# Kernel optimization log

Measured on AMD Instinct MI355X. Metric: run time of the kernel, lower is better.

The kernel has to match this reference:

```python
import jax, jax.numpy as jnp
import numpy as np

EPS = 1e-5
N_NODES = 100000

def _glorot(key, shape):
    lim = float(np.sqrt(6.0 / (shape[0] + shape[1])))
    return jax.random.uniform(key, shape, jnp.float32, -lim, lim)

def setup_inputs() -> dict:
    key = jax.random.key(0)
    ks = jax.random.split(key, 16)
    x = jax.random.normal(ks[0], (N_NODES, 64), jnp.float32)
    edge_index = jax.random.randint(ks[1], (2, 1600000), 0, N_NODES, jnp.int64)
    chans = [64, 128, 128, 1]
    inp = {"x": x, "edge_index": edge_index}
    for i in range(3):
        ci, co = chans[i], chans[i + 1]
        inp[f"Wl{i}"] = _glorot(ks[2 + 3 * i], (ci, co))
        inp[f"bl{i}"] = jnp.zeros((co,), jnp.float32)
        inp[f"Wr{i}"] = _glorot(ks[3 + 3 * i], (ci, co))
    inp["g0"] = jnp.ones((128,), jnp.float32); inp["be0"] = jnp.zeros((128,), jnp.float32)
    inp["g1"] = jnp.ones((128,), jnp.float32); inp["be1"] = jnp.zeros((128,), jnp.float32)
    inp["wF"] = _glorot(ks[11], (1, 1))
    inp["bF"] = jnp.zeros((1,), jnp.float32)
    return inp

def _sage_conv(x, src, dst, Wl, bl, Wr):
    # mean aggregation over incoming edges (PyG SAGEConv default)
    msg = x[src]                                                   # [E, Cin]
    agg = jax.ops.segment_sum(msg, dst, num_segments=N_NODES)      # [N, Cin]
    cnt = jax.ops.segment_sum(jnp.ones((src.shape[0], 1), x.dtype), dst, num_segments=N_NODES)
    agg = agg / jnp.maximum(cnt, 1.0)
    return agg @ Wl + bl + x @ Wr

def _batchnorm(x, g, b):
    mu = jnp.mean(x, axis=0)
    var = jnp.mean(jnp.square(x - mu), axis=0)  # biased, training-mode BN
    return (x - mu) * jax.lax.rsqrt(var + EPS) * g + b

def reference(x, edge_index, Wl0, bl0, Wr0, Wl1, bl1, Wr1, Wl2, bl2, Wr2, g0, be0, g1, be1, wF, bF):
    src, dst = edge_index[0], edge_index[1]
    h = _sage_conv(x, src, dst, Wl0, bl0, Wr0)
    h = jax.nn.relu(_batchnorm(h, g0, be0))
    h = _sage_conv(h, src, dst, Wl1, bl1, Wr1)
    h = jax.nn.relu(_batchnorm(h, g1, be1))
    h = _sage_conv(h, src, dst, Wl2, bl2, Wr2)        # activation 'None', no BN
    h = h @ wF + bF                                    # final Linear(1,1)
    return jax.nn.sigmoid(h)
```

## Files before the change

kernel.cpp:

```cpp
#include <hip/hip_runtime.h>
#include <math.h>

#define BN_EPS 1e-5f
#define SCAN_CHUNK 4096

typedef __attribute__((ext_vector_type(8))) short bf16x8;
typedef __attribute__((ext_vector_type(4))) float f32x4;

__device__ __forceinline__ unsigned short f2bf(float f) {
    unsigned int u = __float_as_uint(f);
    u = (u + 0x7fffu + ((u >> 16) & 1u)) >> 16;
    return (unsigned short)u;
}
__device__ __forceinline__ float bflo(unsigned int u) { return __uint_as_float(u << 16); }
__device__ __forceinline__ float bfhi(unsigned int u) { return __uint_as_float(u & 0xffff0000u); }

__global__ void to_bf16_k(const float* __restrict__ in, unsigned short* __restrict__ out, int n4) {
    int i = blockIdx.x * blockDim.x + threadIdx.x;
    if (i >= n4) return;
    float4 v = ((const float4*)in)[i];
    ((ushort4*)out)[i] = make_ushort4(f2bf(v.x), f2bf(v.y), f2bf(v.z), f2bf(v.w));
}

__global__ void count_edges_sliced_k(const int* __restrict__ dst, int E,
                                     int* __restrict__ cnt, int nper) {
    const int slice = blockIdx.x & 7;
    const int lo = slice * nper;
    const int hi = lo + nper;
    int i = (blockIdx.x >> 3) * blockDim.x + threadIdx.x;
    int stride = (gridDim.x >> 3) * blockDim.x;
    for (int e = i; e < E; e += stride) {
        int d = dst[e];
        if (d >= lo && d < hi) atomicAdd(&cnt[d], 1);
    }
}

__device__ __forceinline__ int wave_incl_scan(int v, int lane) {
#pragma unroll
    for (int d = 1; d < 64; d <<= 1) {
        int u = __shfl_up(v, d);
        if (lane >= d) v += u;
    }
    return v;
}

__global__ void block_sum_k(const int* __restrict__ cnt, int N, int* __restrict__ bsum) {
    const int t = threadIdx.x;
    const int base = blockIdx.x * SCAN_CHUNK;
    int s = 0;
    for (int i = t; i < SCAN_CHUNK; i += 256) {
        int idx = base + i;
        if (idx < N) s += cnt[idx];
    }
    const int lane = t & 63, wid = t >> 6;
#pragma unroll
    for (int d = 32; d; d >>= 1) s += __shfl_down(s, d);
    __shared__ int ws[4];
    if (lane == 0) ws[wid] = s;
    __syncthreads();
    if (t == 0) bsum[blockIdx.x] = ws[0] + ws[1] + ws[2] + ws[3];
}

__global__ void scan_bsums_k(int* __restrict__ bsum, int nb) {
    int lane = threadIdx.x;
    int v = (lane < nb) ? bsum[lane] : 0;
    int incl = wave_incl_scan(v, lane);
    if (lane < nb) bsum[lane] = incl - v;
}

__global__ void scan_write_k(const int* __restrict__ cnt, const int* __restrict__ bsum, int N,
                             int* __restrict__ off, int* __restrict__ cursor,
                             float* __restrict__ inv) {
    const int t = threadIdx.x;
    const int base = blockIdx.x * SCAN_CHUNK;
    const int idx0 = base + t * 16;
    int pre[16];
    int s = 0;
#pragma unroll
    for (int j = 0; j < 16; ++j) {
        int i = idx0 + j;
        int c = (i < N) ? cnt[i] : 0;
        pre[j] = s;
        s += c;
    }
    const int lane = t & 63, wid = t >> 6;
    int incl = wave_incl_scan(s, lane);
    __shared__ int ws[4];
    if (lane == 63) ws[wid] = incl;
    __syncthreads();
    if (t == 0) {
        int a = 0;
#pragma unroll
        for (int w = 0; w < 4; ++w) { int tmp = ws[w]; ws[w] = a; a += tmp; }
    }
    __syncthreads();
    const int tbase = bsum[blockIdx.x] + (incl - s) + ws[wid];
#pragma unroll
    for (int j = 0; j < 16; ++j) {
        int i = idx0 + j;
        if (i < N) {
            int c = cnt[i];
            int o = tbase + pre[j];
            off[i] = o;
            cursor[i] = o;
            inv[i] = 1.0f / fmaxf((float)c, 1.0f);
        }
    }
}

__global__ void csr_fill_sliced_k(const int* __restrict__ src, const int* __restrict__ dst,
                                  const int* __restrict__ off, int E,
                                  int* __restrict__ cursor, int* __restrict__ csr,
                                  float slice_scale) {
    const int slice = blockIdx.x & 7;
    const int g = blockIdx.x >> 3;
    const int ng = gridDim.x >> 3;
    int i = g * blockDim.x + threadIdx.x;
    int stride = ng * blockDim.x;
    for (int e = i; e < E; e += stride) {
        int d = dst[e];
        int o = off[d];
        int s = (int)((float)o * slice_scale);
        s = s > 7 ? 7 : s;
        if (s == slice) {
            int pos = atomicAdd(&cursor[d], 1);
            csr[pos] = src[e];
        }
    }
}

__global__ void wfrag_build_k(const float* __restrict__ Wl, const float* __restrict__ Wr,
                              int CIN, int KIT, unsigned short* __restrict__ wf) {
    int t = blockIdx.x * blockDim.x + threadIdx.x;
    int lane = t & 63;
    int q = t >> 6;
    if (q >= 8 * KIT) return;
    int kit = q % KIT;
    int ct = q / KIT;
    int col = ct * 16 + (lane & 15);
    bf16x8 v;
#pragma unroll
    for (int j = 0; j < 8; ++j) {
        int kg = kit * 32 + ((lane >> 4) << 3) + j;
        float f = (kg < CIN) ? Wl[(size_t)kg * 128 + col] : Wr[(size_t)(kg - CIN) * 128 + col];
        v[j] = (short)f2bf(f);
    }
    ((bf16x8*)wf)[q * 64 + lane] = v;
}

template<int CIN>
__launch_bounds__(256)
__global__ void fused_sage_k(const unsigned short* __restrict__ feat,
                             const unsigned short* __restrict__ xin,
                             const int* __restrict__ csr, const int* __restrict__ off,
                             const int* __restrict__ endp, const float* __restrict__ inv,
                             const unsigned short* __restrict__ wfrag,
                             const float* __restrict__ bl,
                             unsigned short* __restrict__ outb,
                             float* __restrict__ stats8, int N) {
    constexpr int KT = 2 * CIN;
    constexpr int KIT = KT / 32;
    __shared__ unsigned short sA[32 * KT];

    const int t = threadIdx.x;
    const int lane = t & 63, wave = t >> 6;
    const int rowbase = blockIdx.x * 32;
    const unsigned int* f32p = (const unsigned int*)feat;

    constexpr int CH8 = CIN / 8;
    for (int i = t; i < 32 * CH8; i += 256) {
        int r = i / CH8, q = i % CH8;
        if (rowbase + r < N) {
            uint4 v = ((const uint4*)(xin + (size_t)(rowbase + r) * CIN))[q];
            int byte = ((r * KT + CIN + q * 8) * 2) ^ ((r & 7) << 4);
            *(uint4*)((char*)sA + byte) = v;
        }
    }

#pragma unroll
    for (int rr = 0; rr < 8; ++rr) {
        int r = wave * 8 + rr;
        int n = rowbase + r;
        if (n < N) {
            const int o = off[n], eend = endp[n];
            float a0 = 0.f, a1 = 0.f;
            if constexpr (CIN == 128) {
                int e = o;
                for (; e + 3 < eend; e += 4) {
                    unsigned int u0 = f32p[(size_t)csr[e]     * 64 + lane];
                    unsigned int u1 = f32p[(size_t)csr[e + 1] * 64 + lane];
                    unsigned int u2 = f32p[(size_t)csr[e + 2] * 64 + lane];
                    unsigned int u3 = f32p[(size_t)csr[e + 3] * 64 + lane];
                    a0 += (bflo(u0) + bflo(u1)) + (bflo(u2) + bflo(u3));
                    a1 += (bfhi(u0) + bfhi(u1)) + (bfhi(u2) + bfhi(u3));
                }
                for (; e < eend; ++e) {
                    unsigned int u = f32p[(size_t)csr[e] * 64 + lane];
                    a0 += bflo(u); a1 += bfhi(u);
                }
                float iv = inv[n];
                unsigned int pk = (unsigned int)f2bf(a0 * iv) | ((unsigned int)f2bf(a1 * iv) << 16);
                int byte = ((r * KT + 2 * lane) * 2) ^ ((r & 7) << 4);
                *(unsigned int*)((char*)sA + byte) = pk;
            } else {
                const int c = lane & 31, g = lane >> 5;
                int e = o + g;
                for (; e + 7 < eend; e += 8) {
                    unsigned int u0 = f32p[(size_t)csr[e]     * 32 + c];
                    unsigned int u1 = f32p[(size_t)csr[e + 2] * 32 + c];
                    unsigned int u2 = f32p[(size_t)csr[e + 4] * 32 + c];
                    unsigned int u3 = f32p[(size_t)csr[e + 6] * 32 + c];
                    a0 += (bflo(u0) + bflo(u1)) + (bflo(u2) + bflo(u3));
                    a1 += (bfhi(u0) + bfhi(u1)) + (bfhi(u2) + bfhi(u3));
                }
                for (; e < eend; e += 2) {
                    unsigned int u = f32p[(size_t)csr[e] * 32 + c];
                    a0 += bflo(u); a1 += bfhi(u);
                }
                a0 += __shfl_xor(a0, 32);
                a1 += __shfl_xor(a1, 32);
                if (g == 0) {
                    float iv = inv[n];
                    unsigned int pk = (unsigned int)f2bf(a0 * iv) | ((unsigned int)f2bf(a1 * iv) << 16);
                    int byte = ((r * KT + 2 * c) * 2) ^ ((r & 7) << 4);
                    *(unsigned int*)((char*)sA + byte) = pk;
                }
            }
        }
    }
    __syncthreads();

    f32x4 acc00 = {0.f,0.f,0.f,0.f}, acc01 = acc00, acc10 = acc00, acc11 = acc00;
    const int koff = (lane >> 4) << 4;
    const int swz = (lane & 7) << 4;
    const int base0 = (lane & 15) * KT * 2 + koff;
    const int base1 = (16 + (lane & 15)) * KT * 2 + koff;
    const bf16x8* wf8 = (const bf16x8*)wfrag;
    const int bq0 = (wave * 2 + 0) * KIT;
    const int bq1 = (wave * 2 + 1) * KIT;

#pragma unroll
    for (int kit = 0; kit < KIT; ++kit) {
        bf16x8 fa0 = *(const bf16x8*)((const char*)sA + ((base0 + kit * 64) ^ swz));
        bf16x8 fa1 = *(const bf16x8*)((const char*)sA + ((base1 + kit * 64) ^ swz));
        bf16x8 fb0 = wf8[(bq0 + kit) * 64 + lane];
        bf16x8 fb1 = wf8[(bq1 + kit) * 64 + lane];
        acc00 = __builtin_amdgcn_mfma_f32_16x16x32_bf16(fa0, fb0, acc00, 0, 0, 0);
        acc01 = __builtin_amdgcn_mfma_f32_16x16x32_bf16(fa0, fb1, acc01, 0, 0, 0);
        acc10 = __builtin_amdgcn_mfma_f32_16x16x32_bf16(fa1, fb0, acc10, 0, 0, 0);
        acc11 = __builtin_amdgcn_mfma_f32_16x16x32_bf16(fa1, fb1, acc11, 0, 0, 0);
    }

    const int c0 = wave * 32 + (lane & 15);
    const int c1 = c0 + 16;
    const float b0 = bl[c0], b1 = bl[c1];
    float sum0 = 0.f, sq0 = 0.f, sum1 = 0.f, sq1 = 0.f;
    const int row0base = rowbase + ((lane >> 4) << 2);
#pragma unroll
    for (int r = 0; r < 4; ++r) {
        int row0 = row0base + r, row1 = row0 + 16;
        float v00 = acc00[r] + b0, v01 = acc01[r] + b1;
        float v10 = acc10[r] + b0, v11 = acc11[r] + b1;
        if (row0 < N) {
            outb[(size_t)row0 * 128 + c0] = f2bf(v00);
            outb[(size_t)row0 * 128 + c1] = f2bf(v01);
            sum0 += v00; sq0 += v00 * v00; sum1 += v01; sq1 += v01 * v01;
        }
        if (row1 < N) {
            outb[(size_t)row1 * 128 + c0] = f2bf(v10);
            outb[(size_t)row1 * 128 + c1] = f2bf(v11);
            sum0 += v10; sq0 += v10 * v10; sum1 += v11; sq1 += v11 * v11;
        }
    }
#pragma unroll
    for (int m = 16; m < 64; m <<= 1) {
        sum0 += __shfl_xor(sum0, m); sq0 += __shfl_xor(sq0, m);
        sum1 += __shfl_xor(sum1, m); sq1 += __shfl_xor(sq1, m);
    }
    if (lane < 16) {
        float* st = stats8 + (blockIdx.x & 7) * 256;
        atomicAdd(&st[c0], sum0);
        atomicAdd(&st[128 + c0], sq0);
        atomicAdd(&st[c1], sum1);
        atomicAdd(&st[128 + c1], sq1);
    }
}

__global__ void bn_finalize8_k(const float* __restrict__ g, const float* __restrict__ be,
                               const float* __restrict__ stats8, float* __restrict__ sfin, int N) {
    int c = threadIdx.x;
    if (c < 128) {
        float s = 0.f, s2 = 0.f;
#pragma unroll
        for (int k = 0; k < 8; ++k) { s += stats8[k * 256 + c]; s2 += stats8[k * 256 + 128 + c]; }
        float mu = s / (float)N;
        float var = s2 / (float)N - mu * mu;
        float sc = g[c] * rsqrtf(var + BN_EPS);
        sfin[c] = sc;
        sfin[128 + c] = be[c] - mu * sc;
    }
}

__global__ void bn_apply_inplace_k(unsigned short* __restrict__ hb, const float* __restrict__ sfin,
                                   int total_u4) {
    int i = blockIdx.x * blockDim.x + threadIdx.x;
    int stride = gridDim.x * blockDim.x;
    for (; i < total_u4; i += stride) {
        uint4 v = ((uint4*)hb)[i];
        int c0 = (i & 15) * 8;
        unsigned int w[4] = {v.x, v.y, v.z, v.w};
#pragma unroll
        for (int j = 0; j < 4; ++j) {
            float lo = fmaxf(bflo(w[j]) * sfin[c0 + 2*j]     + sfin[128 + c0 + 2*j],     0.f);
            float hi = fmaxf(bfhi(w[j]) * sfin[c0 + 2*j + 1] + sfin[128 + c0 + 2*j + 1], 0.f);
            w[j] = (unsigned int)f2bf(lo) | ((unsigned int)f2bf(hi) << 16);
        }
        ((uint4*)hb)[i] = make_uint4(w[0], w[1], w[2], w[3]);
    }
}

__global__ void bn_apply_p_k(unsigned short* __restrict__ hb, const float* __restrict__ sfin,
                             const float* __restrict__ Wl2, float* __restrict__ p, int N) {
    const int lane = threadIdx.x & 63;
    const int n = (int)((blockIdx.x * (long long)blockDim.x + threadIdx.x) >> 6);
    if (n >= N) return;
    const float2 sc = ((const float2*)sfin)[lane];
    const float2 sh = ((const float2*)(sfin + 128))[lane];
    const float2 w  = ((const float2*)Wl2)[lane];
    unsigned int u = ((unsigned int*)(hb + (size_t)n * 128))[lane];
    float vx = fmaxf(bflo(u) * sc.x + sh.x, 0.f);
    float vy = fmaxf(bfhi(u) * sc.y + sh.y, 0.f);
    ((unsigned int*)(hb + (size_t)n * 128))[lane] = (unsigned int)f2bf(vx) | ((unsigned int)f2bf(vy) << 16);
    float s = vx * w.x + vy * w.y;
#pragma unroll
    for (int o = 32; o; o >>= 1) s += __shfl_down(s, o);
    if (lane == 0) p[n] = s;
}

__global__ void layer2_final_k(const unsigned short* __restrict__ hb, const float* __restrict__ p,
                               const int* __restrict__ csr, const int* __restrict__ off,
                               const int* __restrict__ endp, const float* __restrict__ inv,
                               const float* __restrict__ Wr2, const float* __restrict__ bl2,
                               const float* __restrict__ wF, const float* __restrict__ bF,
                               float* __restrict__ out, int N) {
    const int lane = threadIdx.x & 63;
    const int n = (int)((blockIdx.x * (long long)blockDim.x + threadIdx.x) >> 6);
    if (n >= N) return;
    float2 w = ((const float2*)Wr2)[lane];
    unsigned int u = ((const unsigned int*)(hb + (size_t)n * 128))[lane];
    float dotp = bflo(u) * w.x + bfhi(u) * w.y;
    float ps = 0.f;
    const int o = off[n], e_end = endp[n];
    for (int e = o + lane; e < e_end; e += 64) ps += p[csr[e]];
    float s = dotp + ps * inv[n];
#pragma unroll
    for (int ow = 32; ow; ow >>= 1) s += __shfl_down(s, ow);
    if (lane == 0) {
        float z = (s + bl2[0]) * wF[0] + bF[0];
        out[n] = 1.f / (1.f + expf(-z));
    }
}

extern "C" void kernel_launch(void* const* d_in, const int* in_sizes, int n_in,
                              void* d_out, int out_size, void* d_ws, size_t ws_size,
                              hipStream_t stream) {
    const float* x   = (const float*)d_in[0];
    const int*   ei  = (const int*)d_in[1];
    const int E = in_sizes[1] / 2;
    const int N = in_sizes[0] / 64;
    const int* src = ei;
    const int* dst = ei + E;
    const float* Wl0 = (const float*)d_in[2];
    const float* bl0 = (const float*)d_in[3];
    const float* Wr0 = (const float*)d_in[4];
    const float* Wl1 = (const float*)d_in[5];
    const float* bl1 = (const float*)d_in[6];
    const float* Wr1 = (const float*)d_in[7];
    const float* Wl2 = (const float*)d_in[8];
    const float* bl2 = (const float*)d_in[9];
    const float* Wr2 = (const float*)d_in[10];
    const float* g0  = (const float*)d_in[11];
    const float* be0 = (const float*)d_in[12];
    const float* g1  = (const float*)d_in[13];
    const float* be1 = (const float*)d_in[14];
    const float* wF  = (const float*)d_in[15];
    const float* bF  = (const float*)d_in[16];

    char* wp = (char*)d_ws;
    unsigned short* h0   = (unsigned short*)wp;  wp += (size_t)N * 128 * 2;
    unsigned short* h1   = (unsigned short*)wp;  wp += (size_t)N * 128 * 2;
    unsigned short* xb   = (unsigned short*)wp;  wp += (size_t)N * 64 * 2;
    int*   cnt    = (int*)wp;    wp += (size_t)N * 4;
    int*   off    = (int*)wp;    wp += (size_t)N * 4;
    int*   cursor = (int*)wp;    wp += (size_t)N * 4;
    float* inv    = (float*)wp;  wp += (size_t)N * 4;
    int*   csr    = (int*)wp;    wp += (size_t)E * 4;
    float* stats8a = (float*)wp; wp += 2048 * 4;
    float* stats8b = (float*)wp; wp += 2048 * 4;
    float* sfin0   = (float*)wp; wp += 256 * 4;
    float* sfin1   = (float*)wp; wp += 256 * 4;
    int*   bsum    = (int*)wp;   wp += 64 * 4;
    unsigned short* wf0 = (unsigned short*)wp; wp += 8 * 4 * 64 * 8 * 2;
    unsigned short* wf1 = (unsigned short*)wp; wp += 8 * 8 * 64 * 8 * 2;
    float* p = (float*)cnt;
    float* out = (float*)d_out;

    const int gemm_grid = (N + 31) / 32;
    const int wave_grid = (N + 3) / 4;
    const int nb = (N + SCAN_CHUNK - 1) / SCAN_CHUNK;

    wfrag_build_k<<<(8 * 4 * 64 + 255) / 256, 256, 0, stream>>>(Wl0, Wr0, 64, 4, wf0);
    wfrag_build_k<<<(8 * 8 * 64 + 255) / 256, 256, 0, stream>>>(Wl1, Wr1, 128, 8, wf1);
    to_bf16_k<<<(N * 16 + 255) / 256, 256, 0, stream>>>(x, xb, N * 16);
    hipMemsetAsync(stats8a, 0, (2048 + 2048 + 256 + 256) * sizeof(float), stream);

    hipMemsetAsync(cnt, 0, (size_t)N * sizeof(int), stream);
    count_edges_sliced_k<<<2048, 256, 0, stream>>>(dst, E, cnt, (N + 7) / 8);
    block_sum_k<<<nb, 256, 0, stream>>>(cnt, N, bsum);
    scan_bsums_k<<<1, 64, 0, stream>>>(bsum, nb);
    scan_write_k<<<nb, 256, 0, stream>>>(cnt, bsum, N, off, cursor, inv);
    csr_fill_sliced_k<<<2048, 256, 0, stream>>>(src, dst, off, E, cursor, csr, 8.0f / (float)E);

    fused_sage_k<64><<<gemm_grid, 256, 0, stream>>>(xb, xb, csr, off, cursor, inv,
                                                    wf0, bl0, h0, stats8a, N);
    bn_finalize8_k<<<1, 128, 0, stream>>>(g0, be0, stats8a, sfin0, N);
    bn_apply_inplace_k<<<2048, 256, 0, stream>>>(h0, sfin0, N * 16);

    fused_sage_k<128><<<gemm_grid, 256, 0, stream>>>(h0, h0, csr, off, cursor, inv,
                                                     wf1, bl1, h1, stats8b, N);
    bn_finalize8_k<<<1, 128, 0, stream>>>(g1, be1, stats8b, sfin1, N);
    bn_apply_p_k<<<wave_grid, 256, 0, stream>>>(h1, sfin1, Wl2, p, N);

    layer2_final_k<<<wave_grid, 256, 0, stream>>>(h1, p, csr, off, cursor, inv,
                                                  Wr2, bl2, wF, bF, out, N);
}
```

Measured before the change: 433.8 us.

## Fuse BN0 finalize and apply into layer-1 gather, merge scan kernels

Folds the first BatchNorm finalize and ReLU into the layer-1 fused SAGE kernel, so normalization is applied on the fly to gathered neighbor features and self features. This removes the separate finalize and in-place apply passes over h0. The separate block-sum scan kernel is also merged into scan_write_k, and the gather loops are unrolled to 8 loads with two accumulator pairs. The cost is extra FMA and max work per gathered element (16 edges per node), since BN is now recomputed per edge instead of once per node, plus a redundant stats reduction in every block.

```diff
diff --git a/kernel.cpp b/kernel.cpp
--- a/kernel.cpp
+++ b/kernel.cpp
@@ -14,6 +14,18 @@
 }
 __device__ __forceinline__ float bflo(unsigned int u) { return __uint_as_float(u << 16); }
 __device__ __forceinline__ float bfhi(unsigned int u) { return __uint_as_float(u & 0xffff0000u); }
+
+template<bool BNIN>
+__device__ __forceinline__ void acc2(unsigned int u, float sc0, float sh0, float sc1, float sh1,
+                                     float& a0, float& a1) {
+    if constexpr (BNIN) {
+        a0 += fmaxf(bflo(u) * sc0 + sh0, 0.f);
+        a1 += fmaxf(bfhi(u) * sc1 + sh1, 0.f);
+    } else {
+        a0 += bflo(u);
+        a1 += bfhi(u);
+    }
+}
 
 __global__ void to_bf16_k(const float* __restrict__ in, unsigned short* __restrict__ out, int n4) {
     int i = blockIdx.x * blockDim.x + threadIdx.x;
@@ -61,17 +73,17 @@
     if (t == 0) bsum[blockIdx.x] = ws[0] + ws[1] + ws[2] + ws[3];
 }
 
-__global__ void scan_bsums_k(int* __restrict__ bsum, int nb) {
-    int lane = threadIdx.x;
-    int v = (lane < nb) ? bsum[lane] : 0;
-    int incl = wave_incl_scan(v, lane);
-    if (lane < nb) bsum[lane] = incl - v;
-}
-
-__global__ void scan_write_k(const int* __restrict__ cnt, const int* __restrict__ bsum, int N,
-                             int* __restrict__ off, int* __restrict__ cursor,
+__global__ void scan_write_k(const int* __restrict__ cnt, const int* __restrict__ bsum, int nb,
+                             int N, int* __restrict__ off, int* __restrict__ cursor,
                              float* __restrict__ inv) {
     const int t = threadIdx.x;
+    __shared__ int ws[4];
+    __shared__ int base_s;
+    if (t < 64) {
+        int v = (t < nb) ? bsum[t] : 0;
+        int incl = wave_incl_scan(v, t);
+        if (t == blockIdx.x) base_s = incl - v;
+    }
     const int base = blockIdx.x * SCAN_CHUNK;
     const int idx0 = base + t * 16;
     int pre[16];
@@ -85,7 +97,6 @@
     }
     const int lane = t & 63, wid = t >> 6;
     int incl = wave_incl_scan(s, lane);
-    __shared__ int ws[4];
     if (lane == 63) ws[wid] = incl;
     __syncthreads();
     if (t == 0) {
@@ -94,7 +105,7 @@
         for (int w = 0; w < 4; ++w) { int tmp = ws[w]; ws[w] = a; a += tmp; }
     }
     __syncthreads();
-    const int tbase = bsum[blockIdx.x] + (incl - s) + ws[wid];
+    const int tbase = base_s + (incl - s) + ws[wid];
 #pragma unroll
     for (int j = 0; j < 16; ++j) {
         int i = idx0 + j;
@@ -148,7 +159,7 @@
     ((bf16x8*)wf)[q * 64 + lane] = v;
 }
 
-template<int CIN>
+template<int CIN, bool BNIN>
 __launch_bounds__(256)
 __global__ void fused_sage_k(const unsigned short* __restrict__ feat,
                              const unsigned short* __restrict__ xin,
@@ -156,25 +167,60 @@
                              const int* __restrict__ endp, const float* __restrict__ inv,
                              const unsigned short* __restrict__ wfrag,
                              const float* __restrict__ bl,
+                             const float* __restrict__ g, const float* __restrict__ be,
+                             const float* __restrict__ stats8in,
                              unsigned short* __restrict__ outb,
-                             float* __restrict__ stats8, int N) {
+                             float* __restrict__ stats8out, int N) {
     constexpr int KT = 2 * CIN;
     constexpr int KIT = KT / 32;
     __shared__ unsigned short sA[32 * KT];
+    __shared__ float sfinS[256];
 
     const int t = threadIdx.x;
     const int lane = t & 63, wave = t >> 6;
     const int rowbase = blockIdx.x * 32;
     const unsigned int* f32p = (const unsigned int*)feat;
+
+    if constexpr (BNIN) {
+        if (t < 128) {
+            float s = 0.f, s2 = 0.f;
+#pragma unroll
+            for (int k = 0; k < 8; ++k) { s += stats8in[k * 256 + t]; s2 += stats8in[k * 256 + 128 + t]; }
+            float mu = s / (float)N;
+            float var = s2 / (float)N - mu * mu;
+            float sc = g[t] * rsqrtf(var + BN_EPS);
+            sfinS[t] = sc;
+            sfinS[128 + t] = be[t] - mu * sc;
+        }
+        __syncthreads();
+    }
 
     constexpr int CH8 = CIN / 8;
     for (int i = t; i < 32 * CH8; i += 256) {
         int r = i / CH8, q = i % CH8;
         if (rowbase + r < N) {
             uint4 v = ((const uint4*)(xin + (size_t)(rowbase + r) * CIN))[q];
+            if constexpr (BNIN) {
+                unsigned int w[4] = {v.x, v.y, v.z, v.w};
+#pragma unroll
+                for (int j = 0; j < 4; ++j) {
+                    int c = q * 8 + 2 * j;
+                    float lo = fmaxf(bflo(w[j]) * sfinS[c]     + sfinS[128 + c],     0.f);
+                    float hi = fmaxf(bfhi(w[j]) * sfinS[c + 1] + sfinS[128 + c + 1], 0.f);
+                    w[j] = (unsigned int)f2bf(lo) | ((unsigned int)f2bf(hi) << 16);
+                }
+                v = make_uint4(w[0], w[1], w[2], w[3]);
+            }
             int byte = ((r * KT + CIN + q * 8) * 2) ^ ((r & 7) << 4);
             *(uint4*)((char*)sA + byte) = v;
         }
+    }
+
+    float sc0 = 1.f, sh0 = 0.f, sc1 = 1.f, sh1 = 0.f;
+    if constexpr (BNIN) {
+        int cc = (CIN == 128) ? (2 * lane) : (2 * (lane & 31));
+        sc0 = sfinS[cc];     sh0 = sfinS[128 + cc];
+        sc1 = sfinS[cc + 1]; sh1 = sfinS[128 + cc + 1];
     }
 
 #pragma unroll
@@ -183,43 +229,85 @@
         int n = rowbase + r;
         if (n < N) {
             const int o = off[n], eend = endp[n];
-            float a0 = 0.f, a1 = 0.f;
+            float a0 = 0.f, a1 = 0.f, b0f = 0.f, b1f = 0.f;
             if constexpr (CIN == 128) {
                 int e = o;
+                for (; e + 7 < eend; e += 8) {
+                    unsigned int u0 = f32p[(size_t)csr[e]     * 64 + lane];
+                    unsigned int u1 = f32p[(size_t)csr[e + 1] * 64 + lane];
+                    unsigned int u2 = f32p[(size_t)csr[e + 2] * 64 + lane];
+                    unsigned int u3 = f32p[(size_t)csr[e + 3] * 64 + lane];
+                    unsigned int u4 = f32p[(size_t)csr[e + 4] * 64 + lane];
+                    unsigned int u5 = f32p[(size_t)csr[e + 5] * 64 + lane];
+                    unsigned int u6 = f32p[(size_t)csr[e + 6] * 64 + lane];
+                    unsigned int u7 = f32p[(size_t)csr[e + 7] * 64 + lane];
+                    acc2<BNIN>(u0, sc0, sh0, sc1, sh1, a0, a1);
+                    acc2<BNIN>(u1, sc0, sh0, sc1, sh1, b0f, b1f);
+                    acc2<BNIN>(u2, sc0, sh0, sc1, sh1, a0, a1);
+                    acc2<BNIN>(u3, sc0, sh0, sc1, sh1, b0f, b1f);
+                    acc2<BNIN>(u4, sc0, sh0, sc1, sh1, a0, a1);
+                    acc2<BNIN>(u5, sc0, sh0, sc1, sh1, b0f, b1f);
+                    acc2<BNIN>(u6, sc0, sh0, sc1, sh1, a0, a1);
+                    acc2<BNIN>(u7, sc0, sh0, sc1, sh1, b0f, b1f);
+                }
                 for (; e + 3 < eend; e += 4) {
                     unsigned int u0 = f32p[(size_t)csr[e]     * 64 + lane];
                     unsigned int u1 = f32p[(size_t)csr[e + 1] * 64 + lane];
                     unsigned int u2 = f32p[(size_t)csr[e + 2] * 64 + lane];
                     unsigned int u3 = f32p[(size_t)csr[e + 3] * 64 + lane];
-                    a0 += (bflo(u0) + bflo(u1)) + (bflo(u2) + bflo(u3));
-                    a1 += (bfhi(u0) + bfhi(u1)) + (bfhi(u2) + bfhi(u3));
+                    acc2<BNIN>(u0, sc0, sh0, sc1, sh1, a0, a1);
+                    acc2<BNIN>(u1, sc0, sh0, sc1, sh1, b0f, b1f);
+                    acc2<BNIN>(u2, sc0, sh0, sc1, sh1, a0, a1);
+                    acc2<BNIN>(u3, sc0, sh0, sc1, sh1, b0f, b1f);
                 }
                 for (; e < eend; ++e) {
                     unsigned int u = f32p[(size_t)csr[e] * 64 + lane];
-                    a0 += bflo(u); a1 += bfhi(u);
-                }
+                    acc2<BNIN>(u, sc0, sh0, sc1, sh1, a0, a1);
+                }
+                a0 += b0f; a1 += b1f;
                 float iv = inv[n];
                 unsigned int pk = (unsigned int)f2bf(a0 * iv) | ((unsigned int)f2bf(a1 * iv) << 16);
                 int byte = ((r * KT + 2 * lane) * 2) ^ ((r & 7) << 4);
                 *(unsigned int*)((char*)sA + byte) = pk;
             } else {
-                const int c = lane & 31, g = lane >> 5;
-                int e = o + g;
-                for (; e + 7 < eend; e += 8) {
+                const int c = lane & 31, g2 = lane >> 5;
+                int e = o + g2;
+                for (; e + 14 < eend; e += 16) {
+                    unsigned int u0 = f32p[(size_t)csr[e]      * 32 + c];
+                    unsigned int u1 = f32p[(size_t)csr[e + 2]  * 32 + c];
+                    unsigned int u2 = f32p[(size_t)csr[e + 4]  * 32 + c];
+                    unsigned int u3 = f32p[(size_t)csr[e + 6]  * 32 + c];
+                    unsigned int u4 = f32p[(size_t)csr[e + 8]  * 32 + c];
+                    unsigned int u5 = f32p[(size_t)csr[e + 10] * 32 + c];
+                    unsigned int u6 = f32p[(size_t)csr[e + 12] * 32 + c];
+                    unsigned int u7 = f32p[(size_t)csr[e + 14] * 32 + c];
+                    acc2<false>(u0, 0, 0, 0, 0, a0, a1);
+                    acc2<false>(u1, 0, 0, 0, 0, b0f, b1f);
+                    acc2<false>(u2, 0, 0, 0, 0, a0, a1);
+                    acc2<false>(u3, 0, 0, 0, 0, b0f, b1f);
+                    acc2<false>(u4, 0, 0, 0, 0, a0, a1);
+                    acc2<false>(u5, 0, 0, 0, 0, b0f, b1f);
+                    acc2<false>(u6, 0, 0, 0, 0, a0, a1);
+                    acc2<false>(u7, 0, 0, 0, 0, b0f, b1f);
+                }
+                for (; e + 6 < eend; e += 8) {
                     unsigned int u0 = f32p[(size_t)csr[e]     * 32 + c];
                     unsigned int u1 = f32p[(size_t)csr[e + 2] * 32 + c];
                     unsigned int u2 = f32p[(size_t)csr[e + 4] * 32 + c];
                     unsigned int u3 = f32p[(size_t)csr[e + 6] * 32 + c];
-                    a0 += (bflo(u0) + bflo(u1)) + (bflo(u2) + bflo(u3));
-                    a1 += (bfhi(u0) + bfhi(u1)) + (bfhi(u2) + bfhi(u3));
+                    acc2<false>(u0, 0, 0, 0, 0, a0, a1);
+                    acc2<false>(u1, 0, 0, 0, 0, b0f, b1f);
+                    acc2<false>(u2, 0, 0, 0, 0, a0, a1);
+                    acc2<false>(u3, 0, 0, 0, 0, b0f, b1f);
                 }
                 for (; e < eend; e += 2) {
                     unsigned int u = f32p[(size_t)csr[e] * 32 + c];
-                    a0 += bflo(u); a1 += bfhi(u);
-                }
+                    acc2<false>(u, 0, 0, 0, 0, a0, a1);
+                }
+                a0 += b0f; a1 += b1f;
                 a0 += __shfl_xor(a0, 32);
                 a1 += __shfl_xor(a1, 32);
-                if (g == 0) {
+                if (g2 == 0) {
                     float iv = inv[n];
                     unsigned int pk = (unsigned int)f2bf(a0 * iv) | ((unsigned int)f2bf(a1 * iv) << 16);
                     int byte = ((r * KT + 2 * c) * 2) ^ ((r & 7) << 4);
@@ -278,7 +366,7 @@
         sum1 += __shfl_xor(sum1, m); sq1 += __shfl_xor(sq1, m);
     }
     if (lane < 16) {
-        float* st = stats8 + (blockIdx.x & 7) * 256;
+        float* st = stats8out + (blockIdx.x & 7) * 256;
         atomicAdd(&st[c0], sum0);
         atomicAdd(&st[128 + c0], sq0);
         atomicAdd(&st[c1], sum1);
@@ -298,24 +386,6 @@
         float sc = g[c] * rsqrtf(var + BN_EPS);
         sfin[c] = sc;
         sfin[128 + c] = be[c] - mu * sc;
-    }
-}
-
-__global__ void bn_apply_inplace_k(unsigned short* __restrict__ hb, const float* __restrict__ sfin,
-                                   int total_u4) {
-    int i = blockIdx.x * blockDim.x + threadIdx.x;
-    int stride = gridDim.x * blockDim.x;
-    for (; i < total_u4; i += stride) {
-        uint4 v = ((uint4*)hb)[i];
-        int c0 = (i & 15) * 8;
-        unsigned int w[4] = {v.x, v.y, v.z, v.w};
-#pragma unroll
-        for (int j = 0; j < 4; ++j) {
-            float lo = fmaxf(bflo(w[j]) * sfin[c0 + 2*j]     + sfin[128 + c0 + 2*j],     0.f);
-            float hi = fmaxf(bfhi(w[j]) * sfin[c0 + 2*j + 1] + sfin[128 + c0 + 2*j + 1], 0.f);
-            w[j] = (unsigned int)f2bf(lo) | ((unsigned int)f2bf(hi) << 16);
-        }
-        ((uint4*)hb)[i] = make_uint4(w[0], w[1], w[2], w[3]);
     }
 }
 
@@ -397,7 +467,6 @@
     int*   csr    = (int*)wp;    wp += (size_t)E * 4;
     float* stats8a = (float*)wp; wp += 2048 * 4;
     float* stats8b = (float*)wp; wp += 2048 * 4;
-    float* sfin0   = (float*)wp; wp += 256 * 4;
     float* sfin1   = (float*)wp; wp += 256 * 4;
     int*   bsum    = (int*)wp;   wp += 64 * 4;
     unsigned short* wf0 = (unsigned short*)wp; wp += 8 * 4 * 64 * 8 * 2;
@@ -412,22 +481,20 @@
     wfrag_build_k<<<(8 * 4 * 64 + 255) / 256, 256, 0, stream>>>(Wl0, Wr0, 64, 4, wf0);
     wfrag_build_k<<<(8 * 8 * 64 + 255) / 256, 256, 0, stream>>>(Wl1, Wr1, 128, 8, wf1);
     to_bf16_k<<<(N * 16 + 255) / 256, 256, 0, stream>>>(x, xb, N * 16);
-    hipMemsetAsync(stats8a, 0, (2048 + 2048 + 256 + 256) * sizeof(float), stream);
+    hipMemsetAsync(stats8a, 0, (2048 + 2048) * sizeof(float), stream);
 
     hipMemsetAsync(cnt, 0, (size_t)N * sizeof(int), stream);
     count_edges_sliced_k<<<2048, 256, 0, stream>>>(dst, E, cnt, (N + 7) / 8);
     block_sum_k<<<nb, 256, 0, stream>>>(cnt, N, bsum);
-    scan_bsums_k<<<1, 64, 0, stream>>>(bsum, nb);
-    scan_write_k<<<nb, 256, 0, stream>>>(cnt, bsum, N, off, cursor, inv);
+    scan_write_k<<<nb, 256, 0, stream>>>(cnt, bsum, nb, N, off, cursor, inv);
     csr_fill_sliced_k<<<2048, 256, 0, stream>>>(src, dst, off, E, cursor, csr, 8.0f / (float)E);
 
-    fused_sage_k<64><<<gemm_grid, 256, 0, stream>>>(xb, xb, csr, off, cursor, inv,
-                                                    wf0, bl0, h0, stats8a, N);
-    bn_finalize8_k<<<1, 128, 0, stream>>>(g0, be0, stats8a, sfin0, N);
-    bn_apply_inplace_k<<<2048, 256, 0, stream>>>(h0, sfin0, N * 16);
-
-    fused_sage_k<128><<<gemm_grid, 256, 0, stream>>>(h0, h0, csr, off, cursor, inv,
-                                                     wf1, bl1, h1, stats8b, N);
+    fused_sage_k<64, false><<<gemm_grid, 256, 0, stream>>>(
+        xb, xb, csr, off, cursor, inv, wf0, bl0, nullptr, nullptr, nullptr, h0, stats8a, N);
+
+    fused_sage_k<128, true><<<gemm_grid, 256, 0, stream>>>(
+        h0, h0, csr, off, cursor, inv, wf1, bl1, g0, be0, stats8a, h1, stats8b, N);
+
     bn_finalize8_k<<<1, 128, 0, stream>>>(g1, be1, stats8b, sfin1, N);
     bn_apply_p_k<<<wave_grid, 256, 0, stream>>>(h1, sfin1, Wl2, p, N);
 
```

Result: faster. 397.3 us (-8.4%).
